# Kernel optimization log

Measured on AMD Instinct MI355X. Metric: run time of the kernel, lower is better.

## Reference

```python
import jax, jax.numpy as jnp
import numpy as np

N_NODES = 50000
N_EDGES = 800000
F_IN = 512
HIDDEN = 128
N_CLASSES = 40


def setup_inputs() -> dict:
    key = jax.random.key(0)
    ks = jax.random.split(key, 5)
    x = jax.random.normal(ks[0], (N_NODES, F_IN), dtype=jnp.float32)
    edge_index = jax.random.randint(ks[1], (2, N_EDGES), 0, N_NODES, dtype=jnp.int32)
    # Glorot-ish init for GCNConv linear weights, zero bias (PyG default bias=True)
    W1 = jax.random.normal(ks[2], (F_IN, HIDDEN), dtype=jnp.float32) * (1.0 / np.sqrt(F_IN))
    b1 = jnp.zeros((HIDDEN,), dtype=jnp.float32)
    W2 = jax.random.normal(ks[3], (HIDDEN, N_CLASSES), dtype=jnp.float32) * (1.0 / np.sqrt(HIDDEN))
    b2 = jnp.zeros((N_CLASSES,), dtype=jnp.float32)
    return {"x": x, "edge_index": edge_index, "W1": W1, "b1": b1, "W2": W2, "b2": b2}


def _gcn_conv(x, W, b, row, col, n_nodes):
    """PyG GCNConv: linear transform, then symmetric-normalized aggregation.

    row/col already include self-loops. deg computed over col (in-degree),
    norm = d^{-1/2}[row] * d^{-1/2}[col], out[row] += norm * h[col].
    """
    h = x @ W  # [N, out]
    ones = jnp.ones(col.shape[0], dtype=h.dtype)
    deg = jax.ops.segment_sum(ones, col, num_segments=n_nodes)  # >=1 due to self-loops
    dinv = jax.lax.rsqrt(deg)
    norm = dinv[row] * dinv[col]  # [E]
    msgs = h[col] * norm[:, None]  # [E, out] gather + scale
    out = jax.ops.segment_sum(msgs, row, num_segments=n_nodes)  # scatter-add
    return out + b


def reference(x, edge_index, W1, b1, W2, b2):
    n = x.shape[0]
    loop = jnp.arange(n, dtype=edge_index.dtype)
    row = jnp.concatenate([edge_index[0], loop])
    col = jnp.concatenate([edge_index[1], loop])
    h = _gcn_conv(x, W1, b1, row, col, n)
    h = jax.nn.relu(h)
    # dropout with training=False is identity (eval-mode reference)
    out = _gcn_conv(h, W2, b2, row, col, n)
    return out
```

## Files before the change

kernel.cpp:

```cpp
#include <hip/hip_runtime.h>
#include <hip/hip_bf16.h>

#define N_NODES 50000
#define N_EDGES 800000
#define F_IN 512
#define HIDDEN 128
#define N_CLASSES 40
#define NSCAN 196
#define CB 391

typedef __attribute__((ext_vector_type(4))) float f32x4;
typedef __attribute__((ext_vector_type(8))) short s16x8;

__device__ __forceinline__ unsigned bf16r(float f) {
    unsigned u = __float_as_uint(f);
    return (u + 0x7fffu + ((u >> 16) & 1u)) >> 16;
}
__device__ __forceinline__ unsigned pkbf(float lo, float hi) {
    return bf16r(lo) | (bf16r(hi) << 16);
}
__device__ __forceinline__ float bflo(unsigned u) { return __uint_as_float(u << 16); }
__device__ __forceinline__ float bfhi(unsigned u) { return __uint_as_float(u & 0xffff0000u); }

__global__ void prep_kernel(const float* __restrict__ W1, const float* __restrict__ W2,
                            uint4* __restrict__ w1f, uint4* __restrict__ w2f) {
    int f = blockIdx.x * 256 + threadIdx.x;
    if (f < 8192) {
        int lane = f & 63, u = (f >> 6) & 7, c = f >> 9;
        int k0 = c * 32 + ((lane >> 4) << 3), n = u * 16 + (lane & 15);
        float v[8];
        #pragma unroll
        for (int j = 0; j < 8; ++j) v[j] = W1[(size_t)(k0 + j) * HIDDEN + n];
        uint4 o;
        o.x = pkbf(v[0], v[1]); o.y = pkbf(v[2], v[3]);
        o.z = pkbf(v[4], v[5]); o.w = pkbf(v[6], v[7]);
        w1f[f] = o;
    } else if (f < 8960) {
        int g = f - 8192;
        int lane = g & 63, u = (g >> 6) % 3, c = g / 192;
        int k0 = c * 32 + ((lane >> 4) << 3), n = u * 16 + (lane & 15);
        float v[8];
        #pragma unroll
        for (int j = 0; j < 8; ++j)
            v[j] = (n < N_CLASSES) ? W2[(size_t)(k0 + j) * N_CLASSES + n] : 0.0f;
        uint4 o;
        o.x = pkbf(v[0], v[1]); o.y = pkbf(v[2], v[3]);
        o.z = pkbf(v[4], v[5]); o.w = pkbf(v[6], v[7]);
        w2f[g] = o;
    }
}

__global__ __launch_bounds__(256) void fused_kernel(
    const float* __restrict__ x, const uint4* __restrict__ w1f,
    unsigned short* __restrict__ h1s,
    const int* __restrict__ row, const int* __restrict__ col,
    int* __restrict__ rowcnt, int* __restrict__ colcnt, int* __restrict__ pos8)
{
    __shared__ uint4 XAf[256];

    if (blockIdx.x < CB) {
        const int t = blockIdx.x * 256 + threadIdx.x;
        #pragma unroll
        for (int j = 0; j < 8; ++j) {
            const int e = t + j * (CB * 256);
            if (e < N_EDGES) {
                pos8[e] = atomicAdd(&rowcnt[row[e]], 1);
                atomicAdd(&colcnt[col[e]], 1);
            }
        }
        return;
    }

    const int q = blockIdx.x - CB;
    const int tid  = threadIdx.x;
    const int wave = tid >> 6, lane = tid & 63;
    const int l16  = lane & 15, quad = lane >> 4;
    const int row0 = q * 64;

    f32x4 acc[4][2] = {};

    int sr = row0 + wave * 16 + l16;
    if (sr >= N_NODES) sr = N_NODES - 1;
    const float* xrow = x + (size_t)sr * F_IN + (quad << 3);

    for (int c = 0; c < F_IN / 32; ++c) {
        float4 a = *(const float4*)(xrow + c * 32);
        float4 b = *(const float4*)(xrow + c * 32 + 4);
        uint4 fr;
        fr.x = pkbf(a.x, a.y); fr.y = pkbf(a.z, a.w);
        fr.z = pkbf(b.x, b.y); fr.w = pkbf(b.z, b.w);
        XAf[tid] = fr;
        __syncthreads();

        uint4 t0 = w1f[(size_t)(c * 8 + wave * 2 + 0) * 64 + lane];
        uint4 t1 = w1f[(size_t)(c * 8 + wave * 2 + 1) * 64 + lane];
        s16x8 bf0 = *(s16x8*)&t0, bf1 = *(s16x8*)&t1;

        #pragma unroll
        for (int i = 0; i < 4; ++i) {
            uint4 ta = XAf[i * 64 + lane];
            s16x8 af = *(s16x8*)&ta;
            acc[i][0] = __builtin_amdgcn_mfma_f32_16x16x32_bf16(af, bf0, acc[i][0], 0, 0, 0);
            acc[i][1] = __builtin_amdgcn_mfma_f32_16x16x32_bf16(af, bf1, acc[i][1], 0, 0, 0);
        }
        __syncthreads();
    }

    const int n0 = wave * 32;
    #pragma unroll
    for (int i = 0; i < 4; ++i) {
        #pragma unroll
        for (int p = 0; p < 4; ++p) {
            int gr = row0 + i * 16 + quad * 4 + p;
            if (gr < N_NODES) {
                #pragma unroll
                for (int u = 0; u < 2; ++u)
                    h1s[(size_t)gr * HIDDEN + n0 + u * 16 + l16] =
                        (unsigned short)bf16r(acc[i][u][p]);
            }
        }
    }
}

__global__ void scan_blocks_kernel(const int* __restrict__ rowcnt,
                                   const int* __restrict__ colcnt,
                                   float* __restrict__ dinv,
                                   int* __restrict__ rowptr, int* __restrict__ partials) {
    __shared__ int s[256];
    const int tid = threadIdx.x;
    const int i = blockIdx.x * 256 + tid;
    const int v = (i < N_NODES) ? rowcnt[i] : 0;
    s[tid] = v;
    __syncthreads();
    #pragma unroll
    for (int off = 1; off < 256; off <<= 1) {
        int t = (tid >= off) ? s[tid - off] : 0;
        __syncthreads();
        s[tid] += t;
        __syncthreads();
    }
    if (i < N_NODES) {
        rowptr[i] = s[tid] - v;
        dinv[i] = rsqrtf(1.0f + (float)colcnt[i]);
    }
    if (tid == 255) partials[blockIdx.x] = s[255];
}

__global__ void scan_add_kernel(int* __restrict__ rowptr, const int* __restrict__ partials) {
    __shared__ int s[256];
    const int tid = threadIdx.x;
    s[tid] = (tid < blockIdx.x) ? partials[tid] : 0;
    __syncthreads();
    #pragma unroll
    for (int off = 128; off > 0; off >>= 1) {
        if (tid < off) s[tid] += s[tid + off];
        __syncthreads();
    }
    const int base = s[0];
    const int i = blockIdx.x * 256 + tid;
    if (i < N_NODES) rowptr[i] += base;
    if (i == 0) rowptr[N_NODES] = N_EDGES;
}

__global__ void place_kernel(const int* __restrict__ row, const int* __restrict__ col,
                             const int* __restrict__ rowptr, const int* __restrict__ pos8,
                             int* __restrict__ ecol) {
    int e = blockIdx.x * 256 + threadIdx.x;
    if (e < N_EDGES) ecol[rowptr[row[e]] + pos8[e]] = col[e];
}

__global__ __launch_bounds__(256) void gather1_kernel(
    const int* __restrict__ rowptr, const int* __restrict__ ecol,
    const float* __restrict__ dinv, const unsigned* __restrict__ h1u,
    const float* __restrict__ b1, unsigned* __restrict__ agg1u)
{
    const int wave = threadIdx.x >> 6, lane = threadIdx.x & 63;
    const int r = blockIdx.x * 4 + wave;
    if (r >= N_NODES) return;
    const int start = rowptr[r], end = rowptr[r + 1];

    float ax = 0.f, ay = 0.f, bx = 0.f, by = 0.f;
    float cx = 0.f, cy = 0.f, dx = 0.f, dy = 0.f;
    if (start < end) {
        for (int e = start; e < end; e += 4) {
            const int i1 = min(e + 1, end - 1), i2 = min(e + 2, end - 1), i3 = min(e + 3, end - 1);
            const int c0 = ecol[e], c1 = ecol[i1], c2 = ecol[i2], c3 = ecol[i3];
            const float d0 = dinv[c0];
            const float d1 = (e + 1 < end) ? dinv[c1] : 0.f;
            const float d2 = (e + 2 < end) ? dinv[c2] : 0.f;
            const float d3 = (e + 3 < end) ? dinv[c3] : 0.f;
            unsigned u0 = h1u[(size_t)c0 * 64 + lane];
            unsigned u1 = h1u[(size_t)c1 * 64 + lane];
            unsigned u2 = h1u[(size_t)c2 * 64 + lane];
            unsigned u3 = h1u[(size_t)c3 * 64 + lane];
            ax = fmaf(bflo(u0), d0, ax); ay = fmaf(bfhi(u0), d0, ay);
            bx = fmaf(bflo(u1), d1, bx); by = fmaf(bfhi(u1), d1, by);
            cx = fmaf(bflo(u2), d2, cx); cy = fmaf(bfhi(u2), d2, cy);
            dx = fmaf(bflo(u3), d3, dx); dy = fmaf(bfhi(u3), d3, dy);
        }
    }
    const float s = dinv[r];
    unsigned us = h1u[(size_t)r * 64 + lane];
    float sx = (ax + bx) + (cx + dx) + bflo(us) * s;
    float sy = (ay + by) + (cy + dy) + bfhi(us) * s;
    const float2 bb = *(const float2*)&b1[lane * 2];
    float ox = fmaxf(fmaf(s, sx, bb.x), 0.f);
    float oy = fmaxf(fmaf(s, sy, bb.y), 0.f);
    agg1u[(size_t)r * 64 + lane] = pkbf(ox, oy);
}

__global__ __launch_bounds__(256) void gemm2_kernel(
    const uint4* __restrict__ agg1q, const uint4* __restrict__ w2f,
    const float* __restrict__ dinv, unsigned short* __restrict__ h2b)
{
    __shared__ uint4 XAf[512];
    const int tid  = threadIdx.x;
    const int wave = tid >> 6, lane = tid & 63;
    const int l16  = lane & 15, quad = lane >> 4;
    const int row0 = blockIdx.x * 128;

    f32x4 acc[2][3] = {};

    int r1 = row0 + wave * 16 + l16;        if (r1 >= N_NODES) r1 = N_NODES - 1;
    int r2 = row0 + (4 + wave) * 16 + l16;  if (r2 >= N_NODES) r2 = N_NODES - 1;

    for (int c = 0; c < 4; ++c) {
        XAf[tid]       = agg1q[(size_t)r1 * 16 + c * 4 + quad];
        XAf[tid + 256] = agg1q[(size_t)r2 * 16 + c * 4 + quad];
        __syncthreads();

        s16x8 bf[3];
        #pragma unroll
        for (int u = 0; u < 3; ++u) {
            uint4 t = w2f[(size_t)(c * 3 + u) * 64 + lane];
            bf[u] = *(s16x8*)&t;
        }
        #pragma unroll
        for (int i = 0; i < 2; ++i) {
            uint4 ta = XAf[(wave * 2 + i) * 64 + lane];
            s16x8 af = *(s16x8*)&ta;
            #pragma unroll
            for (int u = 0; u < 3; ++u)
                acc[i][u] = __builtin_amdgcn_mfma_f32_16x16x32_bf16(af, bf[u], acc[i][u], 0, 0, 0);
        }
        __syncthreads();
    }

    #pragma unroll
    for (int i = 0; i < 2; ++i) {
        #pragma unroll
        for (int p = 0; p < 4; ++p) {
            int gr = row0 + (wave * 2 + i) * 16 + quad * 4 + p;
            if (gr < N_NODES) {
                float s = dinv[gr];
                #pragma unroll
                for (int u = 0; u < 3; ++u) {
                    int ncol = u * 16 + l16;
                    if (ncol < N_CLASSES)
                        h2b[(size_t)gr * N_CLASSES + ncol] =
                            (unsigned short)bf16r(acc[i][u][p] * s);
                }
            }
        }
    }
}

__global__ __launch_bounds__(256) void gather2_kernel(
    const int* __restrict__ rowptr, const int* __restrict__ ecol,
    const float* __restrict__ dinv, const unsigned* __restrict__ h2u,
    const float* __restrict__ b2, float* __restrict__ out)
{
    const int wave = threadIdx.x >> 6, lane = threadIdx.x & 63;
    const int r = blockIdx.x * 4 + wave;
    if (r >= N_NODES) return;
    const int g = lane / 20;
    const int j = lane - g * 20;
    const int start = rowptr[r], end = rowptr[r + 1];

    float sx = 0.f, sy = 0.f;
    if (g < 3 && start < end) {
        for (int e = start; e < end; e += 3) {
            const int ee = e + g;
            const int c = ecol[min(ee, end - 1)];
            unsigned u = h2u[(size_t)c * 20 + j];
            u = (ee < end) ? u : 0u;
            sx += bflo(u); sy += bfhi(u);
        }
    }
    float tx = sx + __shfl(sx, lane + 20, 64) + __shfl(sx, lane + 40, 64);
    float ty = sy + __shfl(sy, lane + 20, 64) + __shfl(sy, lane + 40, 64);
    if (lane < 20) {
        unsigned us = h2u[(size_t)r * 20 + j];
        tx += bflo(us); ty += bfhi(us);
        const float2 bb = *(const float2*)&b2[2 * j];
        float2 o;
        o.x = fmaf(dinv[r], tx, bb.x);
        o.y = fmaf(dinv[r], ty, bb.y);
        *(float2*)&out[(size_t)r * N_CLASSES + 2 * j] = o;
    }
}

extern "C" void kernel_launch(void* const* d_in, const int* in_sizes, int n_in,
                              void* d_out, int out_size, void* d_ws, size_t ws_size,
                              hipStream_t stream)
{
    const float* x  = (const float*)d_in[0];
    const int*   ei = (const int*)d_in[1];
    const float* W1 = (const float*)d_in[2];
    const float* b1 = (const float*)d_in[3];
    const float* W2 = (const float*)d_in[4];
    const float* b2 = (const float*)d_in[5];
    const int* row = ei;
    const int* col = ei + N_EDGES;

    float* ws = (float*)d_ws;
    int*   rowcnt   = (int*)(ws);
    int*   colcnt   = (int*)(ws + 65536);
    float* dinv     = ws + 131072;
    int*   rowptr   = (int*)(ws + 196608);
    int*   partials = (int*)(ws + 262144);
    int*   pos8     = (int*)(ws + 270336);
    int*   ecol     = (int*)(ws + 1089536);
    uint4* w1f      = (uint4*)(ws + 1908736);
    uint4* w2f      = (uint4*)(ws + 1941504);
    unsigned short* h1s = (unsigned short*)(ws + 1944576);
    unsigned*       h1u = (unsigned*)h1s;
    unsigned* agg1u = (unsigned*)(ws + 5144576);
    uint4*    agg1q = (uint4*)agg1u;
    unsigned short* h2b = (unsigned short*)(ws + 8344576);
    unsigned*       h2u = (unsigned*)h2b;
    float*    out   = (float*)d_out;

    hipMemsetAsync(rowcnt, 0, 2 * 65536 * sizeof(int), stream);
    prep_kernel<<<35, 256, 0, stream>>>(W1, W2, w1f, w2f);

    fused_kernel<<<CB + 782, 256, 0, stream>>>(x, w1f, h1s, row, col, rowcnt, colcnt, pos8);

    scan_blocks_kernel<<<NSCAN, 256, 0, stream>>>(rowcnt, colcnt, dinv, rowptr, partials);
    scan_add_kernel<<<NSCAN, 256, 0, stream>>>(rowptr, partials);
    place_kernel<<<3125, 256, 0, stream>>>(row, col, rowptr, pos8, ecol);

    gather1_kernel<<<N_NODES / 4, 256, 0, stream>>>(rowptr, ecol, dinv, h1u, b1, agg1u);
    gemm2_kernel<<<(N_NODES + 127) / 128, 256, 0, stream>>>(agg1q, w2f, dinv, h2b);
    gather2_kernel<<<N_NODES / 4, 256, 0, stream>>>(rowptr, ecol, dinv, h2u, b2, out);
}
```

Measured before the change: 332.1 us.

## Replace global col-degree atomics with LDS sliced histograms; unroll gather to 8 edges

Column in-degree counting moves from global atomicAdd into 512 extra blocks. Each block builds a 16-bit-packed LDS histogram over one edge slice and one eighth of the node range, then writes it to scratch, and the scan kernel sums the 64 slices per node. This removes half of the global atomics in the fused kernel. The cost is extra scratch traffic, each col slice being read 8 times, and a 64-way reduction in the scan. The gather1 loop also handles 8 edges per iteration with independent accumulators for more memory-level parallelism.

```diff
diff --git a/kernel.cpp b/kernel.cpp
--- a/kernel.cpp
+++ b/kernel.cpp
@@ -7,7 +7,13 @@
 #define HIDDEN 128
 #define N_CLASSES 40
 #define NSCAN 196
+
 #define CB 391
+#define NSLICE 64
+#define SLICE_E 12500
+#define EIGHTH_N 6250
+#define HB (NSLICE*8)
+#define GB 782
 
 typedef __attribute__((ext_vector_type(4))) float f32x4;
 typedef __attribute__((ext_vector_type(8))) short s16x8;
@@ -54,24 +60,43 @@
     const float* __restrict__ x, const uint4* __restrict__ w1f,
     unsigned short* __restrict__ h1s,
     const int* __restrict__ row, const int* __restrict__ col,
-    int* __restrict__ rowcnt, int* __restrict__ colcnt, int* __restrict__ pos8)
-{
-    __shared__ uint4 XAf[256];
+    int* __restrict__ rowcnt, int* __restrict__ pos8,
+    unsigned* __restrict__ scratch32)
+{
+    __shared__ __align__(16) unsigned lds_u[3200];
 
     if (blockIdx.x < CB) {
         const int t = blockIdx.x * 256 + threadIdx.x;
         #pragma unroll
         for (int j = 0; j < 8; ++j) {
             const int e = t + j * (CB * 256);
-            if (e < N_EDGES) {
-                pos8[e] = atomicAdd(&rowcnt[row[e]], 1);
-                atomicAdd(&colcnt[col[e]], 1);
-            }
+            if (e < N_EDGES) pos8[e] = atomicAdd(&rowcnt[row[e]], 1);
         }
         return;
     }
 
-    const int q = blockIdx.x - CB;
+    if (blockIdx.x < CB + HB) {
+        const int hb = blockIdx.x - CB;
+        const int s  = hb & (NSLICE - 1);
+        const int q  = hb >> 6;
+        const int lo = q * EIGHTH_N;
+        for (int i = threadIdx.x; i < EIGHTH_N / 2; i += 256) lds_u[i] = 0u;
+        __syncthreads();
+        const int e0 = s * SLICE_E;
+        for (int i = threadIdx.x; i < SLICE_E; i += 256) {
+            const int c = col[e0 + i];
+            const int lc = c - lo;
+            if ((unsigned)lc < (unsigned)EIGHTH_N)
+                atomicAdd(&lds_u[lc >> 1], 1u << ((lc & 1) * 16));
+        }
+        __syncthreads();
+        unsigned* dst = scratch32 + (size_t)s * (N_NODES / 2) + q * (EIGHTH_N / 2);
+        for (int w = threadIdx.x; w < EIGHTH_N / 2; w += 256) dst[w] = lds_u[w];
+        return;
+    }
+
+    uint4* XAf = (uint4*)lds_u;
+    const int q = blockIdx.x - CB - HB;
     const int tid  = threadIdx.x;
     const int wave = tid >> 6, lane = tid & 63;
     const int l16  = lane & 15, quad = lane >> 4;
@@ -123,7 +148,7 @@
 }
 
 __global__ void scan_blocks_kernel(const int* __restrict__ rowcnt,
-                                   const int* __restrict__ colcnt,
+                                   const unsigned short* __restrict__ scratch16,
                                    float* __restrict__ dinv,
                                    int* __restrict__ rowptr, int* __restrict__ partials) {
     __shared__ int s[256];
@@ -141,7 +166,11 @@
     }
     if (i < N_NODES) {
         rowptr[i] = s[tid] - v;
-        dinv[i] = rsqrtf(1.0f + (float)colcnt[i]);
+        unsigned deg = 0;
+        #pragma unroll 8
+        for (int sl = 0; sl < NSLICE; ++sl)
+            deg += scratch16[(size_t)sl * N_NODES + i];
+        dinv[i] = rsqrtf(1.0f + (float)deg);
     }
     if (tid == 255) partials[blockIdx.x] = s[255];
 }
@@ -179,30 +208,29 @@
     if (r >= N_NODES) return;
     const int start = rowptr[r], end = rowptr[r + 1];
 
-    float ax = 0.f, ay = 0.f, bx = 0.f, by = 0.f;
-    float cx = 0.f, cy = 0.f, dx = 0.f, dy = 0.f;
+    float accx[8] = {}, accy[8] = {};
     if (start < end) {
-        for (int e = start; e < end; e += 4) {
-            const int i1 = min(e + 1, end - 1), i2 = min(e + 2, end - 1), i3 = min(e + 3, end - 1);
-            const int c0 = ecol[e], c1 = ecol[i1], c2 = ecol[i2], c3 = ecol[i3];
-            const float d0 = dinv[c0];
-            const float d1 = (e + 1 < end) ? dinv[c1] : 0.f;
-            const float d2 = (e + 2 < end) ? dinv[c2] : 0.f;
-            const float d3 = (e + 3 < end) ? dinv[c3] : 0.f;
-            unsigned u0 = h1u[(size_t)c0 * 64 + lane];
-            unsigned u1 = h1u[(size_t)c1 * 64 + lane];
-            unsigned u2 = h1u[(size_t)c2 * 64 + lane];
-            unsigned u3 = h1u[(size_t)c3 * 64 + lane];
-            ax = fmaf(bflo(u0), d0, ax); ay = fmaf(bfhi(u0), d0, ay);
-            bx = fmaf(bflo(u1), d1, bx); by = fmaf(bfhi(u1), d1, by);
-            cx = fmaf(bflo(u2), d2, cx); cy = fmaf(bfhi(u2), d2, cy);
-            dx = fmaf(bflo(u3), d3, dx); dy = fmaf(bfhi(u3), d3, dy);
+        for (int e = start; e < end; e += 8) {
+            int cs[8]; float ds[8]; unsigned us[8];
+            #pragma unroll
+            for (int j = 0; j < 8; ++j) cs[j] = ecol[min(e + j, end - 1)];
+            #pragma unroll
+            for (int j = 0; j < 8; ++j) ds[j] = (e + j < end) ? dinv[cs[j]] : 0.f;
+            #pragma unroll
+            for (int j = 0; j < 8; ++j) us[j] = h1u[(size_t)cs[j] * 64 + lane];
+            #pragma unroll
+            for (int j = 0; j < 8; ++j) {
+                accx[j] = fmaf(bflo(us[j]), ds[j], accx[j]);
+                accy[j] = fmaf(bfhi(us[j]), ds[j], accy[j]);
+            }
         }
     }
     const float s = dinv[r];
-    unsigned us = h1u[(size_t)r * 64 + lane];
-    float sx = (ax + bx) + (cx + dx) + bflo(us) * s;
-    float sy = (ay + by) + (cy + dy) + bfhi(us) * s;
+    unsigned uself = h1u[(size_t)r * 64 + lane];
+    float sx = ((accx[0] + accx[1]) + (accx[2] + accx[3])) +
+               ((accx[4] + accx[5]) + (accx[6] + accx[7])) + bflo(uself) * s;
+    float sy = ((accy[0] + accy[1]) + (accy[2] + accy[3])) +
+               ((accy[4] + accy[5]) + (accy[6] + accy[7])) + bfhi(uself) * s;
     const float2 bb = *(const float2*)&b1[lane * 2];
     float ox = fmaxf(fmaf(s, sx, bb.x), 0.f);
     float oy = fmaxf(fmaf(s, sy, bb.y), 0.f);
@@ -315,28 +343,30 @@
 
     float* ws = (float*)d_ws;
     int*   rowcnt   = (int*)(ws);
-    int*   colcnt   = (int*)(ws + 65536);
-    float* dinv     = ws + 131072;
-    int*   rowptr   = (int*)(ws + 196608);
-    int*   partials = (int*)(ws + 262144);
-    int*   pos8     = (int*)(ws + 270336);
-    int*   ecol     = (int*)(ws + 1089536);
-    uint4* w1f      = (uint4*)(ws + 1908736);
-    uint4* w2f      = (uint4*)(ws + 1941504);
-    unsigned short* h1s = (unsigned short*)(ws + 1944576);
+    float* dinv     = ws + 65536;
+    int*   rowptr   = (int*)(ws + 131072);
+    int*   partials = (int*)(ws + 196608);
+    int*   pos8     = (int*)(ws + 204800);
+    int*   ecol     = (int*)(ws + 1024000);
+    unsigned* scratch32 = (unsigned*)(ws + 1843200);
+    unsigned short* scratch16 = (unsigned short*)scratch32;
+    uint4* w1f      = (uint4*)(ws + 3443200);
+    uint4* w2f      = (uint4*)(ws + 3475968);
+    unsigned short* h1s = (unsigned short*)(ws + 3479040);
     unsigned*       h1u = (unsigned*)h1s;
-    unsigned* agg1u = (unsigned*)(ws + 5144576);
+    unsigned* agg1u = (unsigned*)(ws + 6679040);
     uint4*    agg1q = (uint4*)agg1u;
-    unsigned short* h2b = (unsigned short*)(ws + 8344576);
+    unsigned short* h2b = (unsigned short*)(ws + 9879040);
     unsigned*       h2u = (unsigned*)h2b;
     float*    out   = (float*)d_out;
 
-    hipMemsetAsync(rowcnt, 0, 2 * 65536 * sizeof(int), stream);
+    hipMemsetAsync(rowcnt, 0, 65536 * sizeof(int), stream);
     prep_kernel<<<35, 256, 0, stream>>>(W1, W2, w1f, w2f);
 
-    fused_kernel<<<CB + 782, 256, 0, stream>>>(x, w1f, h1s, row, col, rowcnt, colcnt, pos8);
-
-    scan_blocks_kernel<<<NSCAN, 256, 0, stream>>>(rowcnt, colcnt, dinv, rowptr, partials);
+    fused_kernel<<<CB + HB + GB, 256, 0, stream>>>(x, w1f, h1s, row, col,
+                                                   rowcnt, pos8, scratch32);
+
+    scan_blocks_kernel<<<NSCAN, 256, 0, stream>>>(rowcnt, scratch16, dinv, rowptr, partials);
     scan_add_kernel<<<NSCAN, 256, 0, stream>>>(rowptr, partials);
     place_kernel<<<3125, 256, 0, stream>>>(row, col, rowptr, pos8, ecol);
 
```

Measured after the change: 310.5 us. 1.07x faster.
